# Kernel tuning notes

Hardware: AMD Instinct MI355X
Metric: run time of the kernel (lower is better)

Reference implementation:

```python
import jax, jax.numpy as jnp
import numpy as np

MAX_SHIFT = 128


def setup_inputs() -> dict:
    key = jax.random.key(0)
    k1, k2 = jax.random.split(key)
    B, T = 128, 4096
    preds = jax.random.normal(k1, (B, T), dtype=jnp.float32)
    labels = jax.random.normal(k2, (B, T), dtype=jnp.float32)
    return {"preds": preds, "labels": labels}


def reference(preds, labels):
    # Pad both signals by max_shift zeros on each side (as in F.pad).
    pad = MAX_SHIFT
    pp = jnp.pad(preds, ((0, 0), (pad, pad)))   # [B, L], L = T + 2*max_shift
    pl = jnp.pad(labels, ((0, 0), (pad, pad)))  # [B, L]
    L = pp.shape[-1]

    # torch.roll(x, shifts=s): out[j] = x[(j - s) mod L]. Build all S circular
    # rolls at once via a gather: idx[s, j] = (j - s) mod L.
    shifts = jnp.arange(-MAX_SHIFT, MAX_SHIFT + 1)          # [S]
    idx = (jnp.arange(L)[None, :] - shifts[:, None]) % L    # [S, L]
    rolled = pp[:, idx]                                     # [B, S, L]

    # Pearson correlation of each rolled preds row against padded labels
    # (equivalent to torch.corrcoef(stack([rolled, labels]))[0, 1]).
    xm = rolled - jnp.mean(rolled, axis=-1, keepdims=True)  # [B, S, L]
    ym = pl - jnp.mean(pl, axis=-1, keepdims=True)          # [B, L]
    cov = jnp.einsum('bsl,bl->bs', xm, ym)                  # [B, S]
    x_norm = jnp.sqrt(jnp.sum(xm * xm, axis=-1))            # [B, S]
    y_norm = jnp.sqrt(jnp.sum(ym * ym, axis=-1))            # [B]
    corr = cov / (x_norm * y_norm[:, None])                 # [B, S]

    # correlations_to_loss (abstract in source) instantiated as the standard
    # choice: 1 - max correlation over shifts; forward returns batch mean.
    loss_per_sample = 1.0 - jnp.max(corr, axis=-1)          # [B]
    return jnp.mean(loss_per_sample)
```

## Files before the change

### kernel.cpp

```cpp
#include <hip/hip_runtime.h>

#define BB   128
#define TT   4096
#define NSH  257
#define PAD  128
#define LTOT 4352.0f
#define TC   2048
#define PPW  (TC + 256)

__device__ __forceinline__ float wave_sum(float v) {
    #pragma unroll
    for (int m = 32; m; m >>= 1) v += __shfl_xor(v, m, 64);
    return v;
}

extern "C" __global__ __launch_bounds__(256)
void k_corr(const float* __restrict__ preds, const float* __restrict__ labels,
            float* __restrict__ cov_g, float* __restrict__ stats_g) {
    __shared__ float pp_s[PPW];
    __shared__ float lab_s[TC];
    __shared__ float cov_s[NSH];

    const int bid = blockIdx.x;
    const int b   = bid >> 1;
    const int t0  = (bid & 1) * TC;
    const int tid = threadIdx.x;

    const float* pr = preds  + b * TT;
    const float* lr = labels + b * TT;

    #pragma unroll
    for (int v = tid; v < PPW; v += 256) {
        int idx = t0 + v - PAD;
        pp_s[v] = (idx >= 0 && idx < TT) ? pr[idx] : 0.0f;
    }
    #pragma unroll
    for (int v = tid; v < TC; v += 256) lab_s[v] = lr[t0 + v];
    for (int j = tid; j < NSH; j += 256) cov_s[j] = 0.0f;
    __syncthreads();

    const int l    = tid & 63;
    const int wv   = tid >> 6;
    const int tq0  = wv * (TC / 4);
    const int boff = 256 - 4 * l;

    float4 prev = *reinterpret_cast<const float4*>(&pp_s[tq0 + boff - 4]);
    float a0 = 0.f, a1 = 0.f, a2 = 0.f, a3 = 0.f;

    #pragma unroll 4
    for (int tq = tq0; tq < tq0 + TC / 4; tq += 4) {
        const float4 lab = *reinterpret_cast<const float4*>(&lab_s[tq]);
        const float4 cur = *reinterpret_cast<const float4*>(&pp_s[tq + boff]);
        a0 += lab.x * cur.x;  a0 += lab.y * cur.y;  a0 += lab.z * cur.z;  a0 += lab.w * cur.w;
        a1 += lab.x * prev.w; a1 += lab.y * cur.x;  a1 += lab.z * cur.y;  a1 += lab.w * cur.z;
        a2 += lab.x * prev.z; a2 += lab.y * prev.w; a2 += lab.z * cur.x;  a2 += lab.w * cur.y;
        a3 += lab.x * prev.y; a3 += lab.y * prev.z; a3 += lab.z * prev.w; a3 += lab.w * cur.x;
        prev = cur;
    }
    atomicAdd(&cov_s[4 * l + 0], a0);
    atomicAdd(&cov_s[4 * l + 1], a1);
    atomicAdd(&cov_s[4 * l + 2], a2);
    atomicAdd(&cov_s[4 * l + 3], a3);

    {
        float e = 0.f;
        const int vb = tid * (TC / 256);
        #pragma unroll
        for (int u = 0; u < TC / 256; ++u) e += lab_s[vb + u] * pp_s[vb + u];
        e = wave_sum(e);
        if (l == 0) atomicAdd(&cov_s[256], e);
    }

    {
        float sp = 0.f, spp = 0.f, sl = 0.f, sll = 0.f;
        #pragma unroll
        for (int v = tid; v < TC; v += 256) {
            float pv = pp_s[v + PAD];
            float lv = lab_s[v];
            sp += pv; spp += pv * pv; sl += lv; sll += lv * lv;
        }
        sp = wave_sum(sp); spp = wave_sum(spp); sl = wave_sum(sl); sll = wave_sum(sll);
        if (l == 0) {
            atomicAdd(&stats_g[b * 4 + 0], sp);
            atomicAdd(&stats_g[b * 4 + 1], spp);
            atomicAdd(&stats_g[b * 4 + 2], sl);
            atomicAdd(&stats_g[b * 4 + 3], sll);
        }
    }

    __syncthreads();
    for (int j = tid; j < NSH; j += 256) atomicAdd(&cov_g[b * NSH + j], cov_s[j]);
}

extern "C" __global__ __launch_bounds__(1024)
void k_final(const float* __restrict__ cov_g, const float* __restrict__ stats_g,
             float* __restrict__ out) {
    __shared__ float part[16];
    const int tid  = threadIdx.x;
    const int lane = tid & 63;
    const int wv   = tid >> 6;

    float sum = 0.f;
    for (int b = wv; b < BB; b += 16) {
        float Sp  = stats_g[b * 4 + 0], Spp = stats_g[b * 4 + 1];
        float Sl  = stats_g[b * 4 + 2], Sll = stats_g[b * 4 + 3];
        float xn2 = Spp - Sp * Sp / LTOT;
        float yn2 = Sll - Sl * Sl / LTOT;
        float inv = rsqrtf(xn2 * yn2);
        float cst = Sp * Sl / LTOT;
        float mx = -1e30f;
        for (int j = lane; j < NSH; j += 64)
            mx = fmaxf(mx, (cov_g[b * NSH + j] - cst) * inv);
        #pragma unroll
        for (int m = 32; m; m >>= 1) mx = fmaxf(mx, __shfl_xor(mx, m, 64));
        sum += 1.0f - mx;
    }
    if (lane == 0) part[wv] = sum;
    __syncthreads();
    if (tid == 0) {
        float t = 0.f;
        #pragma unroll
        for (int w = 0; w < 16; ++w) t += part[w];
        out[0] = t * (1.0f / BB);
    }
}

extern "C" void kernel_launch(void* const* d_in, const int* in_sizes, int n_in,
                              void* d_out, int out_size, void* d_ws, size_t ws_size,
                              hipStream_t stream) {
    const float* preds  = (const float*)d_in[0];
    const float* labels = (const float*)d_in[1];
    float* out     = (float*)d_out;
    float* cov_g   = (float*)d_ws;
    float* stats_g = cov_g + BB * NSH;

    hipMemsetAsync(d_ws, 0, (size_t)(BB * NSH + BB * 4) * sizeof(float), stream);
    hipLaunchKernelGGL(k_corr, dim3(BB * 2), dim3(256), 0, stream,
                       preds, labels, cov_g, stats_g);
    hipLaunchKernelGGL(k_final, dim3(1), dim3(1024), 0, stream,
                       cov_g, stats_g, out);
}
```

Measured before the change: 85.91 us.

## Split rows into four chunks with 1024-thread blocks, drop memset and global atomics

```diff
diff --git a/kernel.cpp b/kernel.cpp
--- a/kernel.cpp
+++ b/kernel.cpp
@@ -5,7 +5,8 @@
 #define NSH  257
 #define PAD  128
 #define LTOT 4352.0f
-#define TC   2048
+#define NCH  4
+#define TC   1024
 #define PPW  (TC + 256)
 
 __device__ __forceinline__ float wave_sum(float v) {
@@ -14,41 +15,43 @@
     return v;
 }
 
-extern "C" __global__ __launch_bounds__(256)
+extern "C" __global__ __launch_bounds__(1024)
 void k_corr(const float* __restrict__ preds, const float* __restrict__ labels,
-            float* __restrict__ cov_g, float* __restrict__ stats_g) {
+            float* __restrict__ cov_ws, float* __restrict__ stats_ws) {
     __shared__ float pp_s[PPW];
     __shared__ float lab_s[TC];
     __shared__ float cov_s[NSH];
+    __shared__ float st_s[4];
 
     const int bid = blockIdx.x;
-    const int b   = bid >> 1;
-    const int t0  = (bid & 1) * TC;
+    const int b   = bid >> 2;
+    const int c   = bid & 3;
+    const int t0  = c * TC;
     const int tid = threadIdx.x;
 
     const float* pr = preds  + b * TT;
     const float* lr = labels + b * TT;
 
     #pragma unroll
-    for (int v = tid; v < PPW; v += 256) {
+    for (int v = tid; v < PPW; v += 1024) {
         int idx = t0 + v - PAD;
         pp_s[v] = (idx >= 0 && idx < TT) ? pr[idx] : 0.0f;
     }
-    #pragma unroll
-    for (int v = tid; v < TC; v += 256) lab_s[v] = lr[t0 + v];
-    for (int j = tid; j < NSH; j += 256) cov_s[j] = 0.0f;
+    lab_s[tid] = lr[t0 + tid];
+    if (tid < NSH) cov_s[tid] = 0.0f;
+    if (tid < 4)   st_s[tid]  = 0.0f;
     __syncthreads();
 
     const int l    = tid & 63;
     const int wv   = tid >> 6;
-    const int tq0  = wv * (TC / 4);
+    const int tq0  = wv * (TC / 16);
     const int boff = 256 - 4 * l;
 
     float4 prev = *reinterpret_cast<const float4*>(&pp_s[tq0 + boff - 4]);
     float a0 = 0.f, a1 = 0.f, a2 = 0.f, a3 = 0.f;
 
-    #pragma unroll 4
-    for (int tq = tq0; tq < tq0 + TC / 4; tq += 4) {
+    #pragma unroll
+    for (int tq = tq0; tq < tq0 + TC / 16; tq += 4) {
         const float4 lab = *reinterpret_cast<const float4*>(&lab_s[tq]);
         const float4 cur = *reinterpret_cast<const float4*>(&pp_s[tq + boff]);
         a0 += lab.x * cur.x;  a0 += lab.y * cur.y;  a0 += lab.z * cur.z;  a0 += lab.w * cur.w;
@@ -63,37 +66,32 @@
     atomicAdd(&cov_s[4 * l + 3], a3);
 
     {
-        float e = 0.f;
-        const int vb = tid * (TC / 256);
-        #pragma unroll
-        for (int u = 0; u < TC / 256; ++u) e += lab_s[vb + u] * pp_s[vb + u];
-        e = wave_sum(e);
+        float e = wave_sum(lab_s[tid] * pp_s[tid]);
         if (l == 0) atomicAdd(&cov_s[256], e);
     }
 
     {
-        float sp = 0.f, spp = 0.f, sl = 0.f, sll = 0.f;
-        #pragma unroll
-        for (int v = tid; v < TC; v += 256) {
-            float pv = pp_s[v + PAD];
-            float lv = lab_s[v];
-            sp += pv; spp += pv * pv; sl += lv; sll += lv * lv;
-        }
-        sp = wave_sum(sp); spp = wave_sum(spp); sl = wave_sum(sl); sll = wave_sum(sll);
+        float pv = pp_s[tid + PAD];
+        float lv = lab_s[tid];
+        float sp  = wave_sum(pv);
+        float spp = wave_sum(pv * pv);
+        float sl  = wave_sum(lv);
+        float sll = wave_sum(lv * lv);
         if (l == 0) {
-            atomicAdd(&stats_g[b * 4 + 0], sp);
-            atomicAdd(&stats_g[b * 4 + 1], spp);
-            atomicAdd(&stats_g[b * 4 + 2], sl);
-            atomicAdd(&stats_g[b * 4 + 3], sll);
+            atomicAdd(&st_s[0], sp);
+            atomicAdd(&st_s[1], spp);
+            atomicAdd(&st_s[2], sl);
+            atomicAdd(&st_s[3], sll);
         }
     }
 
     __syncthreads();
-    for (int j = tid; j < NSH; j += 256) atomicAdd(&cov_g[b * NSH + j], cov_s[j]);
+    if (tid < NSH) cov_ws[bid * NSH + tid] = cov_s[tid];
+    if (tid < 4)   stats_ws[bid * 4 + tid] = st_s[tid];
 }
 
 extern "C" __global__ __launch_bounds__(1024)
-void k_final(const float* __restrict__ cov_g, const float* __restrict__ stats_g,
+void k_final(const float* __restrict__ cov_ws, const float* __restrict__ stats_ws,
              float* __restrict__ out) {
     __shared__ float part[16];
     const int tid  = threadIdx.x;
@@ -102,15 +100,23 @@
 
     float sum = 0.f;
     for (int b = wv; b < BB; b += 16) {
-        float Sp  = stats_g[b * 4 + 0], Spp = stats_g[b * 4 + 1];
-        float Sl  = stats_g[b * 4 + 2], Sll = stats_g[b * 4 + 3];
+        float Sp = 0.f, Spp = 0.f, Sl = 0.f, Sll = 0.f;
+        #pragma unroll
+        for (int c = 0; c < NCH; ++c) {
+            const float* st = stats_ws + (b * NCH + c) * 4;
+            Sp += st[0]; Spp += st[1]; Sl += st[2]; Sll += st[3];
+        }
         float xn2 = Spp - Sp * Sp / LTOT;
         float yn2 = Sll - Sl * Sl / LTOT;
         float inv = rsqrtf(xn2 * yn2);
         float cst = Sp * Sl / LTOT;
         float mx = -1e30f;
-        for (int j = lane; j < NSH; j += 64)
-            mx = fmaxf(mx, (cov_g[b * NSH + j] - cst) * inv);
+        for (int j = lane; j < NSH; j += 64) {
+            float cv = 0.f;
+            #pragma unroll
+            for (int c = 0; c < NCH; ++c) cv += cov_ws[(b * NCH + c) * NSH + j];
+            mx = fmaxf(mx, (cv - cst) * inv);
+        }
         #pragma unroll
         for (int m = 32; m; m >>= 1) mx = fmaxf(mx, __shfl_xor(mx, m, 64));
         sum += 1.0f - mx;
@@ -130,13 +136,12 @@
                               hipStream_t stream) {
     const float* preds  = (const float*)d_in[0];
     const float* labels = (const float*)d_in[1];
-    float* out     = (float*)d_out;
-    float* cov_g   = (float*)d_ws;
-    float* stats_g = cov_g + BB * NSH;
+    float* out      = (float*)d_out;
+    float* cov_ws   = (float*)d_ws;
+    float* stats_ws = cov_ws + BB * NCH * NSH;
 
-    hipMemsetAsync(d_ws, 0, (size_t)(BB * NSH + BB * 4) * sizeof(float), stream);
-    hipLaunchKernelGGL(k_corr, dim3(BB * 2), dim3(256), 0, stream,
-                       preds, labels, cov_g, stats_g);
+    hipLaunchKernelGGL(k_corr, dim3(BB * NCH), dim3(1024), 0, stream,
+                       preds, labels, cov_ws, stats_ws);
     hipLaunchKernelGGL(k_final, dim3(1), dim3(1024), 0, stream,
-                       cov_g, stats_g, out);
+                       cov_ws, stats_ws, out);
 }
```

Result: slower. 96.85 us (+12.7%).
